# Performance work log

Hardware: AMD Instinct MI355X
Metric: run time of the kernel (lower is better)

Reference implementation:

```python
import jax, jax.numpy as jnp
import numpy as np

N_NODES = 100000


def sage_conv(x, src, dst, W_l, b_l, W_r):
    # PyG SAGEConv (aggr='mean'): out = lin_l(mean_j x_j) + lin_r(x_i)
    msg = x[src]  # [E, d] gather of source-node features
    agg = jax.ops.segment_sum(msg, dst, num_segments=N_NODES)  # [N, d]
    deg = jax.ops.segment_sum(jnp.ones((src.shape[0],), x.dtype), dst,
                              num_segments=N_NODES)
    mean = agg / jnp.clip(deg, 1.0, None)[:, None]
    return mean @ W_l.T + b_l + x @ W_r.T


def setup_inputs() -> dict:
    key = jax.random.key(0)
    ks = jax.random.split(key, 12)
    d_in, d_h, d_out, n_edges = 64, 64, 2, 1200000
    s = 1.0 / np.sqrt(d_h)
    inp = {
        "x": jax.random.normal(ks[0], (N_NODES, d_in), dtype=jnp.float32),
        "edge_index": jax.random.randint(ks[1], (2, n_edges), 0, N_NODES,
                                         dtype=jnp.int64),
        "W_l1": jax.random.uniform(ks[2], (d_h, d_in), jnp.float32, -s, s),
        "b_l1": jax.random.uniform(ks[3], (d_h,), jnp.float32, -s, s),
        "W_r1": jax.random.uniform(ks[4], (d_h, d_in), jnp.float32, -s, s),
        "W_l2": jax.random.uniform(ks[5], (d_h, d_h), jnp.float32, -s, s),
        "b_l2": jax.random.uniform(ks[6], (d_h,), jnp.float32, -s, s),
        "W_r2": jax.random.uniform(ks[7], (d_h, d_h), jnp.float32, -s, s),
        "W_c": jax.random.uniform(ks[8], (d_out, d_h), jnp.float32, -s, s),
        "b_c": jax.random.uniform(ks[9], (d_out,), jnp.float32, -s, s),
    }
    return inp


def reference(x, edge_index, W_l1, b_l1, W_r1, W_l2, b_l2, W_r2, W_c, b_c):
    src, dst = edge_index[0], edge_index[1]
    # layer 1 + relu (dropout is identity in eval mode)
    h = jax.nn.relu(sage_conv(x, src, dst, W_l1, b_l1, W_r1))
    # layer 2 (no relu per forward())
    h = sage_conv(h, src, dst, W_l2, b_l2, W_r2)
    # classifier
    return h @ W_c.T + b_c
```

## Files before the change

### kernel.cpp

```cpp
#include <hip/hip_runtime.h>

#define N_NODES 100000
#define D 64
#define NBUCK 391
#define NBLK_A 512
#define GCNT_N (NBUCK * NBLK_A)
#define NCHUNK ((GCNT_N + 255) / 256)
#define NTILE (N_NODES / 32)

typedef __attribute__((ext_vector_type(8))) short short8;
typedef __attribute__((ext_vector_type(16))) float f32x16;
union Pack8 { uint4 u; short8 s; };

__device__ __forceinline__ unsigned f2bf(float f) {
  unsigned u = __float_as_uint(f);
  return (u + 0x7fffu + ((u >> 16) & 1u)) >> 16;
}
#define BF_LO(u) __uint_as_float(((unsigned)(u)) << 16)
#define BF_HI(u) __uint_as_float(((unsigned)(u)) & 0xffff0000u)


__global__ __launch_bounds__(256) void passA_count(const int* __restrict__ dst,
                                                   int* __restrict__ gcnt,
                                                   int nE, int ec) {
  __shared__ int cnt[NBUCK];
  int t = threadIdx.x, blk = blockIdx.x;
  for (int i = t; i < NBUCK; i += 256) cnt[i] = 0;
  __syncthreads();
  int e0 = blk * ec, e1 = min(e0 + ec, nE);
  for (int e = e0 + t; e < e1; e += 256) atomicAdd(&cnt[dst[e] >> 8], 1);
  __syncthreads();
  for (int b = t; b < NBUCK; b += 256) gcnt[b * NBLK_A + blk] = cnt[b];
}

__global__ void gscan_p1(const int* __restrict__ g, int* __restrict__ csum) {
  int t = threadIdx.x, b = blockIdx.x;
  int i = b * 256 + t;
  int v = (i < GCNT_N) ? g[i] : 0;
  for (int off = 32; off; off >>= 1) v += __shfl_down(v, off);
  __shared__ int ws4[4];
  if ((t & 63) == 0) ws4[t >> 6] = v;
  __syncthreads();
  if (t == 0) csum[b] = ws4[0] + ws4[1] + ws4[2] + ws4[3];
}

__global__ void gscan_p2(int* __restrict__ csum, int nB) {
  __shared__ int s[1024];
  int t = threadIdx.x;
  int orig = (t < nB) ? csum[t] : 0;
  s[t] = orig;
  __syncthreads();
  for (int off = 1; off < 1024; off <<= 1) {
    int v = (t >= off) ? s[t - off] : 0;
    __syncthreads();
    s[t] += v;
    __syncthreads();
  }
  if (t < nB) csum[t] = s[t] - orig;
}

__global__ void gscan_p3(int* __restrict__ g, const int* __restrict__ csum) {
  __shared__ int s[256];
  int t = threadIdx.x, b = blockIdx.x;
  int i = b * 256 + t;
  int d = (i < GCNT_N) ? g[i] : 0;
  s[t] = d;
  __syncthreads();
  for (int off = 1; off < 256; off <<= 1) {
    int v = (t >= off) ? s[t - off] : 0;
    __syncthreads();
    s[t] += v;
    __syncthreads();
  }
  if (i < GCNT_N) g[i] = s[t] - d + csum[b];
}

__global__ __launch_bounds__(256) void passC_place(const int* __restrict__ src,
                                                   const int* __restrict__ dst,
                                                   const int* __restrict__ S,
                                                   uint2* __restrict__ pairs,
                                                   int nE, int ec) {
  __shared__ int cur[NBUCK];
  int t = threadIdx.x, blk = blockIdx.x;
  for (int b = t; b < NBUCK; b += 256) cur[b] = S[b * NBLK_A + blk];
  __syncthreads();
  int e0 = blk * ec, e1 = min(e0 + ec, nE);
  for (int e = e0 + t; e < e1; e += 256) {
    int d = dst[e];
    int p = atomicAdd(&cur[d >> 8], 1);
    pairs[p] = make_uint2((unsigned)d, (unsigned)src[e]);
  }
}

__global__ __launch_bounds__(256) void passD_csr(const uint2* __restrict__ pairs,
                                                 const int* __restrict__ S,
                                                 int* __restrict__ rowstart,
                                                 int* __restrict__ degI,
                                                 int* __restrict__ adj, int nE) {
  __shared__ int lh[256];
  __shared__ int sc[256];
  __shared__ int cur[256];
  int t = threadIdx.x, b = blockIdx.x;
  int base = S[b * NBLK_A];
  int end = (b == NBUCK - 1) ? nE : S[(b + 1) * NBLK_A];
  lh[t] = 0;
  __syncthreads();
  for (int p = base + t; p < end; p += 256) atomicAdd(&lh[pairs[p].x & 255], 1);
  __syncthreads();
  int d = lh[t];
  sc[t] = d;
  __syncthreads();
  for (int off = 1; off < 256; off <<= 1) {
    int v = (t >= off) ? sc[t - off] : 0;
    __syncthreads();
    sc[t] += v;
    __syncthreads();
  }
  int ex = sc[t] - d;
  int node = b * 256 + t;
  if (node < N_NODES) {
    rowstart[node] = base + ex;
    degI[node] = d;
  }
  cur[t] = base + ex;
  __syncthreads();
  for (int p = base + t; p < end; p += 256) {
    uint2 e = pairs[p];
    int slot = atomicAdd(&cur[e.x & 255], 1);
    adj[slot] = (int)e.y;
  }
}

__global__ void wfold_kernel(const float* __restrict__ Wc,
                             const float* __restrict__ Wl2,
                             const float* __restrict__ Wr2,
                             const float* __restrict__ bl2,
                             const float* __restrict__ bc,
                             float* __restrict__ A2, float* __restrict__ B2,
                             float* __restrict__ bfv) {
  int t = threadIdx.x;
  int c = t >> 6, k = t & 63;
  float sa = 0.f, sb = 0.f;
  for (int j = 0; j < 64; ++j) {
    float w = Wc[c * 64 + j];
    sa = fmaf(w, Wl2[j * 64 + k], sa);
    sb = fmaf(w, Wr2[j * 64 + k], sb);
  }
  A2[c * 64 + k] = sa;
  B2[c * 64 + k] = sb;
  if (t < 2) {
    float s = bc[t];
    for (int j = 0; j < 64; ++j) s = fmaf(Wc[t * 64 + j], bl2[j], s);
    bfv[t] = s;
  }
}

__global__ void wprep_kernel(const float* __restrict__ Wl,
                             const float* __restrict__ Wr,
                             unsigned short* __restrict__ wcat) {
  int i = blockIdx.x * 256 + threadIdx.x;
  if (i < 4096) wcat[i] = (unsigned short)f2bf(Wl[i]);
  else if (i < 8192) wcat[i] = (unsigned short)f2bf(Wr[i - 4096]);
}

__global__ __launch_bounds__(256) void transform_mfma(
    const float* __restrict__ x, const unsigned short* __restrict__ wcat,
    const float* __restrict__ bl, unsigned short* __restrict__ t1,
    unsigned short* __restrict__ r1b) {
  int tid = threadIdx.x, lane = tid & 63;
  int l31 = lane & 31, hi = lane >> 5;

  short8 af[4][4];
#pragma unroll
  for (int jt = 0; jt < 4; ++jt)
#pragma unroll
    for (int kk = 0; kk < 4; ++kk)
      af[jt][kk] = *(const short8*)(wcat + (jt * 32 + l31) * 64 + kk * 16 + 8 * hi);

  const f32x16 Z = {0.f, 0.f, 0.f, 0.f, 0.f, 0.f, 0.f, 0.f,
                    0.f, 0.f, 0.f, 0.f, 0.f, 0.f, 0.f, 0.f};
  const float4* x4 = (const float4*)x;

  int gw = (blockIdx.x * 256 + tid) >> 6;
  int nW = (gridDim.x * 256) >> 6;

  for (int tile = gw; tile < NTILE; tile += nW) {
    int node = tile * 32 + l31;
    f32x16 acc[4] = {Z, Z, Z, Z};
#pragma unroll
    for (int kk = 0; kk < 4; ++kk) {
      float4 fa = x4[(size_t)node * 16 + kk * 4 + 2 * hi];
      float4 fb = x4[(size_t)node * 16 + kk * 4 + 2 * hi + 1];
      Pack8 pk;
      pk.u.x = f2bf(fa.x) | (f2bf(fa.y) << 16);
      pk.u.y = f2bf(fa.z) | (f2bf(fa.w) << 16);
      pk.u.z = f2bf(fb.x) | (f2bf(fb.y) << 16);
      pk.u.w = f2bf(fb.z) | (f2bf(fb.w) << 16);
      acc[0] = __builtin_amdgcn_mfma_f32_32x32x16_bf16(af[0][kk], pk.s, acc[0], 0, 0, 0);
      acc[1] = __builtin_amdgcn_mfma_f32_32x32x16_bf16(af[1][kk], pk.s, acc[1], 0, 0, 0);
      acc[2] = __builtin_amdgcn_mfma_f32_32x32x16_bf16(af[2][kk], pk.s, acc[2], 0, 0, 0);
      acc[3] = __builtin_amdgcn_mfma_f32_32x32x16_bf16(af[3][kk], pk.s, acc[3], 0, 0, 0);
    }
#pragma unroll
    for (int jt = 0; jt < 2; ++jt)
#pragma unroll
      for (int rg = 0; rg < 4; ++rg) {
        int j0 = jt * 32 + 8 * rg + 4 * hi;
        uint2 p;
        p.x = f2bf(acc[jt][4 * rg + 0]) | (f2bf(acc[jt][4 * rg + 1]) << 16);
        p.y = f2bf(acc[jt][4 * rg + 2]) | (f2bf(acc[jt][4 * rg + 3]) << 16);
        *(uint2*)(t1 + (size_t)node * 64 + j0) = p;
      }
#pragma unroll
    for (int jt = 2; jt < 4; ++jt)
#pragma unroll
      for (int rg = 0; rg < 4; ++rg) {
        int j0 = (jt - 2) * 32 + 8 * rg + 4 * hi;
        float4 bv = ((const float4*)bl)[j0 >> 2];
        uint2 p;
        p.x = f2bf(acc[jt][4 * rg + 0] + bv.x) |
              (f2bf(acc[jt][4 * rg + 1] + bv.y) << 16);
        p.y = f2bf(acc[jt][4 * rg + 2] + bv.z) |
              (f2bf(acc[jt][4 * rg + 3] + bv.w) << 16);
        *(uint2*)(r1b + (size_t)node * 64 + j0) = p;
      }
  }
}

#define ACC8(acc, v, m)                     \
  acc[0] = fmaf(BF_LO(v.x), m, acc[0]);     \
  acc[1] = fmaf(BF_HI(v.x), m, acc[1]);     \
  acc[2] = fmaf(BF_LO(v.y), m, acc[2]);     \
  acc[3] = fmaf(BF_HI(v.y), m, acc[3]);     \
  acc[4] = fmaf(BF_LO(v.z), m, acc[4]);     \
  acc[5] = fmaf(BF_HI(v.z), m, acc[5]);     \
  acc[6] = fmaf(BF_LO(v.w), m, acc[6]);     \
  acc[7] = fmaf(BF_HI(v.w), m, acc[7]);

__global__ __launch_bounds__(512) void gather1_kernel(
    const int* __restrict__ rowstart, const int* __restrict__ degI,
    const int* __restrict__ adj, const unsigned short* __restrict__ t1,
    const unsigned short* __restrict__ r1b, const float* __restrict__ A2,
    const float* __restrict__ B2, float2* __restrict__ g2,
    float2* __restrict__ s2, int nE) {
  __shared__ float pAB[4][64];
  int tid = threadIdx.x;
  if (tid < 256) {
    int v = tid >> 6, f = tid & 63;
    pAB[v][f] = (v < 2) ? A2[v * 64 + f] : B2[(v - 2) * 64 + f];
  }
  __syncthreads();

  int lane = tid & 63;
  int o = lane >> 3, j8 = lane & 7;
  int gw = (blockIdx.x * 512 + tid) >> 6;
  int nW = (gridDim.x * 512) >> 6;

  for (int n = gw * 2; n < N_NODES; n += nW * 2) {
    int n1 = n + 1;
    int rs0 = rowstart[n], dg0 = degI[n];
    int rs1 = rowstart[n1], dg1 = degI[n1];
    float acc0[8] = {0.f, 0.f, 0.f, 0.f, 0.f, 0.f, 0.f, 0.f};
    float acc1[8] = {0.f, 0.f, 0.f, 0.f, 0.f, 0.f, 0.f, 0.f};
    int mx = max(dg0, dg1);
    for (int base = 0; base < mx; base += 64) {
      int cnt0 = min(max(dg0 - base, 0), 64);
      int cnt1 = min(max(dg1 - base, 0), 64);
      int a0 = adj[min(rs0 + base + ((lane < cnt0) ? lane : 0), nE - 1)];
      int a1 = adj[min(rs1 + base + ((lane < cnt1) ? lane : 0), nE - 1)];
      int mc = max(cnt0, cnt1);
      for (int t = 0; t < mc; t += 16) {
        int el0 = t + o, el1 = t + 8 + o;
        int b00 = __shfl(a0, el0), b01 = __shfl(a0, el1);
        int b10 = __shfl(a1, el0), b11 = __shfl(a1, el1);
        bool k00 = el0 < cnt0, k01 = el1 < cnt0;
        bool k10 = el0 < cnt1, k11 = el1 < cnt1;
        b00 = k00 ? b00 : n;  b01 = k01 ? b01 : n;
        b10 = k10 ? b10 : n1; b11 = k11 ? b11 : n1;
        uint4 v00 = *(const uint4*)(t1 + (size_t)b00 * 64 + j8 * 8);
        uint4 v01 = *(const uint4*)(t1 + (size_t)b01 * 64 + j8 * 8);
        uint4 v10 = *(const uint4*)(t1 + (size_t)b10 * 64 + j8 * 8);
        uint4 v11 = *(const uint4*)(t1 + (size_t)b11 * 64 + j8 * 8);
        float m00 = k00 ? 1.f : 0.f, m01 = k01 ? 1.f : 0.f;
        float m10 = k10 ? 1.f : 0.f, m11 = k11 ? 1.f : 0.f;
        ACC8(acc0, v00, m00)
        ACC8(acc0, v01, m01)
        ACC8(acc1, v10, m10)
        ACC8(acc1, v11, m11)
      }
    }
#pragma unroll
    for (int jj = 0; jj < 8; ++jj) {
      acc0[jj] += __shfl_xor(acc0[jj], 8);
      acc0[jj] += __shfl_xor(acc0[jj], 16);
      acc0[jj] += __shfl_xor(acc0[jj], 32);
      acc1[jj] += __shfl_xor(acc1[jj], 8);
      acc1[jj] += __shfl_xor(acc1[jj], 16);
      acc1[jj] += __shfl_xor(acc1[jj], 32);
    }
#pragma unroll
    for (int nn = 0; nn < 2; ++nn) {
      int nd = nn ? n1 : n;
      float* acc = nn ? acc1 : acc0;
      int dg = nn ? dg1 : dg0;
      float inv = 1.f / (float)max(dg, 1);
      uint4 rv = *(const uint4*)(r1b + (size_t)nd * 64 + j8 * 8);
      float h[8];
      h[0] = fmaxf(fmaf(acc[0], inv, BF_LO(rv.x)), 0.f);
      h[1] = fmaxf(fmaf(acc[1], inv, BF_HI(rv.x)), 0.f);
      h[2] = fmaxf(fmaf(acc[2], inv, BF_LO(rv.y)), 0.f);
      h[3] = fmaxf(fmaf(acc[3], inv, BF_HI(rv.y)), 0.f);
      h[4] = fmaxf(fmaf(acc[4], inv, BF_LO(rv.z)), 0.f);
      h[5] = fmaxf(fmaf(acc[5], inv, BF_HI(rv.z)), 0.f);
      h[6] = fmaxf(fmaf(acc[6], inv, BF_LO(rv.w)), 0.f);
      h[7] = fmaxf(fmaf(acc[7], inv, BF_HI(rv.w)), 0.f);
      float d0 = 0.f, d1 = 0.f, d2 = 0.f, d3 = 0.f;
#pragma unroll
      for (int i = 0; i < 8; ++i) {
        float hv = h[i];
        d0 = fmaf(hv, pAB[0][j8 * 8 + i], d0);
        d1 = fmaf(hv, pAB[1][j8 * 8 + i], d1);
        d2 = fmaf(hv, pAB[2][j8 * 8 + i], d2);
        d3 = fmaf(hv, pAB[3][j8 * 8 + i], d3);
      }
      d0 += __shfl_xor(d0, 1); d0 += __shfl_xor(d0, 2); d0 += __shfl_xor(d0, 4);
      d1 += __shfl_xor(d1, 1); d1 += __shfl_xor(d1, 2); d1 += __shfl_xor(d1, 4);
      d2 += __shfl_xor(d2, 1); d2 += __shfl_xor(d2, 2); d2 += __shfl_xor(d2, 4);
      d3 += __shfl_xor(d3, 1); d3 += __shfl_xor(d3, 2); d3 += __shfl_xor(d3, 4);
      if (lane == 0) {
        g2[nd] = make_float2(d0, d1);
        s2[nd] = make_float2(d2, d3);
      }
    }
  }
}

__global__ __launch_bounds__(256) void gather2_kernel(
    const int* __restrict__ rowstart, const int* __restrict__ degI,
    const int* __restrict__ adj, const float2* __restrict__ g2,
    const float2* __restrict__ s2, const float* __restrict__ bfv,
    float* __restrict__ out, int nE) {
  int tid = threadIdx.x, lane = tid & 63;
  int q = lane >> 4, l16 = lane & 15;
  float bf0 = bfv[0], bf1 = bfv[1];
  int gq = ((blockIdx.x * 256 + tid) >> 6) * 4 + q;
  int strideN = ((gridDim.x * 256) >> 6) * 4;
  for (int n = gq; n < N_NODES; n += strideN) {
    int rs = rowstart[n], dg = degI[n];
    float s0 = 0.f, s1 = 0.f;
    for (int base = 0; base < dg; base += 16) {
      int e = base + l16;
      int a = adj[min(rs + ((e < dg) ? e : 0), nE - 1)];
      float2 v = g2[a];
      float m = (e < dg) ? 1.f : 0.f;
      s0 = fmaf(v.x, m, s0);
      s1 = fmaf(v.y, m, s1);
    }
    s0 += __shfl_xor(s0, 1); s0 += __shfl_xor(s0, 2);
    s0 += __shfl_xor(s0, 4); s0 += __shfl_xor(s0, 8);
    s1 += __shfl_xor(s1, 1); s1 += __shfl_xor(s1, 2);
    s1 += __shfl_xor(s1, 4); s1 += __shfl_xor(s1, 8);
    if (l16 == 0) {
      float inv = 1.f / (float)max(dg, 1);
      float2 sv = s2[n];
      out[(size_t)n * 2 + 0] = fmaf(s0, inv, sv.x) + bf0;
      out[(size_t)n * 2 + 1] = fmaf(s1, inv, sv.y) + bf1;
    }
  }
}

extern "C" void kernel_launch(void* const* d_in, const int* in_sizes, int n_in,
                              void* d_out, int out_size, void* d_ws,
                              size_t ws_size, hipStream_t stream) {
  const float* x   = (const float*)d_in[0];
  const int*   ei  = (const int*)d_in[1];
  const float* Wl1 = (const float*)d_in[2];
  const float* bl1 = (const float*)d_in[3];
  const float* Wr1 = (const float*)d_in[4];
  const float* Wl2 = (const float*)d_in[5];
  const float* bl2 = (const float*)d_in[6];
  const float* Wr2 = (const float*)d_in[7];
  const float* Wc  = (const float*)d_in[8];
  const float* bc  = (const float*)d_in[9];
  float* out = (float*)d_out;

  int nE = in_sizes[1] / 2;
  const int* src = ei;
  const int* dst = ei + nE;

  unsigned short* r1b = (unsigned short*)d_ws;
  uint2* pairs = (uint2*)d_ws;
  unsigned short* t1 = r1b + (size_t)N_NODES * D;
  float2* g2 = (float2*)(t1 + (size_t)N_NODES * D);
  float2* s2 = g2 + N_NODES;
  float* A2 = (float*)(s2 + N_NODES);
  float* B2 = A2 + 128;
  float* bfv = B2 + 128;
  unsigned short* wcat = (unsigned short*)(bfv + 4);
  int* degI = (int*)(wcat + 8192);
  int* rowstart = degI + N_NODES;
  int* gcnt = rowstart + N_NODES;
  int* csum = gcnt + GCNT_N;
  int* adj = csum + 1024;

  int ec = (nE + NBLK_A - 1) / NBLK_A;

  passA_count<<<NBLK_A, 256, 0, stream>>>(dst, gcnt, nE, ec);
  gscan_p1<<<NCHUNK, 256, 0, stream>>>(gcnt, csum);
  gscan_p2<<<1, 1024, 0, stream>>>(csum, NCHUNK);
  gscan_p3<<<NCHUNK, 256, 0, stream>>>(gcnt, csum);
  passC_place<<<NBLK_A, 256, 0, stream>>>(src, dst, gcnt, pairs, nE, ec);
  passD_csr<<<NBUCK, 256, 0, stream>>>(pairs, gcnt, rowstart, degI, adj, nE);

  wfold_kernel<<<1, 128, 0, stream>>>(Wc, Wl2, Wr2, bl2, bc, A2, B2, bfv);
  wprep_kernel<<<32, 256, 0, stream>>>(Wl1, Wr1, wcat);
  transform_mfma<<<512, 256, 0, stream>>>(x, wcat, bl1, t1, r1b);
  gather1_kernel<<<1024, 512, 0, stream>>>(rowstart, degI, adj, t1, r1b, A2,
                                           B2, g2, s2, nE);
  gather2_kernel<<<512, 256, 0, stream>>>(rowstart, degI, adj, g2, s2, bfv,
                                          out, nE);
}
```

Before: 145.7 us.

## Bucket edges by 32-node tiles and aggregate layer 1 with MFMA one-hot matmul

Edge binning now uses 32-node tiles instead of 256-node buckets, so each wave owns one tile's edge list straight from the placed pairs. The layer-1 mean aggregation runs as a bf16 MFMA: gathered neighbor rows are staged in LDS and multiplied by a one-hot destination matrix, replacing per-node CSR gathers with shuffle reductions. This removes the per-node adjacency indirection and shuffle reductions from the gather. In exchange, the count/scan arrays grow about 8x and the counting kernels use fewer blocks with larger shared histograms. Work per tile is also serialized through 16-edge groups with LDS round trips.

```diff
diff --git a/kernel.cpp b/kernel.cpp
--- a/kernel.cpp
+++ b/kernel.cpp
@@ -2,11 +2,13 @@
 
 #define N_NODES 100000
 #define D 64
-#define NBUCK 391
-#define NBLK_A 512
-#define GCNT_N (NBUCK * NBLK_A)
+#define NTILES 3125
+#define NBLK_A 256
+#define GCNT_N (NTILES * NBLK_A)
 #define NCHUNK ((GCNT_N + 255) / 256)
-#define NTILE (N_NODES / 32)
+#define NBUCK_D 391
+#define NTILE_T (N_NODES / 32)
+#define TROW 72
 
 typedef __attribute__((ext_vector_type(8))) short short8;
 typedef __attribute__((ext_vector_type(16))) float f32x16;
@@ -23,14 +25,14 @@
 __global__ __launch_bounds__(256) void passA_count(const int* __restrict__ dst,
                                                    int* __restrict__ gcnt,
                                                    int nE, int ec) {
-  __shared__ int cnt[NBUCK];
+  __shared__ int cnt[NTILES];
   int t = threadIdx.x, blk = blockIdx.x;
-  for (int i = t; i < NBUCK; i += 256) cnt[i] = 0;
+  for (int i = t; i < NTILES; i += 256) cnt[i] = 0;
   __syncthreads();
   int e0 = blk * ec, e1 = min(e0 + ec, nE);
-  for (int e = e0 + t; e < e1; e += 256) atomicAdd(&cnt[dst[e] >> 8], 1);
-  __syncthreads();
-  for (int b = t; b < NBUCK; b += 256) gcnt[b * NBLK_A + blk] = cnt[b];
+  for (int e = e0 + t; e < e1; e += 256) atomicAdd(&cnt[dst[e] >> 5], 1);
+  __syncthreads();
+  for (int b = t; b < NTILES; b += 256) gcnt[b * NBLK_A + blk] = cnt[b];
 }
 
 __global__ void gscan_p1(const int* __restrict__ g, int* __restrict__ csum) {
@@ -47,16 +49,23 @@
 __global__ void gscan_p2(int* __restrict__ csum, int nB) {
   __shared__ int s[1024];
   int t = threadIdx.x;
-  int orig = (t < nB) ? csum[t] : 0;
-  s[t] = orig;
-  __syncthreads();
-  for (int off = 1; off < 1024; off <<= 1) {
-    int v = (t >= off) ? s[t - off] : 0;
-    __syncthreads();
-    s[t] += v;
-    __syncthreads();
-  }
-  if (t < nB) csum[t] = s[t] - orig;
+  int carry = 0;
+  for (int c0 = 0; c0 < nB; c0 += 1024) {
+    int i = c0 + t;
+    int orig = (i < nB) ? csum[i] : 0;
+    s[t] = orig;
+    __syncthreads();
+    for (int off = 1; off < 1024; off <<= 1) {
+      int v = (t >= off) ? s[t - off] : 0;
+      __syncthreads();
+      s[t] += v;
+      __syncthreads();
+    }
+    if (i < nB) csum[i] = s[t] - orig + carry;
+    int tot = s[1023];
+    __syncthreads();
+    carry += tot;
+  }
 }
 
 __global__ void gscan_p3(int* __restrict__ g, const int* __restrict__ csum) {
@@ -80,14 +89,14 @@
                                                    const int* __restrict__ S,
                                                    uint2* __restrict__ pairs,
                                                    int nE, int ec) {
-  __shared__ int cur[NBUCK];
+  __shared__ int cur[NTILES];
   int t = threadIdx.x, blk = blockIdx.x;
-  for (int b = t; b < NBUCK; b += 256) cur[b] = S[b * NBLK_A + blk];
+  for (int b = t; b < NTILES; b += 256) cur[b] = S[b * NBLK_A + blk];
   __syncthreads();
   int e0 = blk * ec, e1 = min(e0 + ec, nE);
   for (int e = e0 + t; e < e1; e += 256) {
     int d = dst[e];
-    int p = atomicAdd(&cur[d >> 8], 1);
+    int p = atomicAdd(&cur[d >> 5], 1);
     pairs[p] = make_uint2((unsigned)d, (unsigned)src[e]);
   }
 }
@@ -101,8 +110,8 @@
   __shared__ int sc[256];
   __shared__ int cur[256];
   int t = threadIdx.x, b = blockIdx.x;
-  int base = S[b * NBLK_A];
-  int end = (b == NBUCK - 1) ? nE : S[(b + 1) * NBLK_A];
+  int base = S[(b * 8) * NBLK_A];
+  int end = (b == NBUCK_D - 1) ? nE : S[((b + 1) * 8) * NBLK_A];
   lh[t] = 0;
   __syncthreads();
   for (int p = base + t; p < end; p += 256) atomicAdd(&lh[pairs[p].x & 255], 1);
@@ -184,7 +193,7 @@
   int gw = (blockIdx.x * 256 + tid) >> 6;
   int nW = (gridDim.x * 256) >> 6;
 
-  for (int tile = gw; tile < NTILE; tile += nW) {
+  for (int tile = gw; tile < NTILE_T; tile += nW) {
     int node = tile * 32 + l31;
     f32x16 acc[4] = {Z, Z, Z, Z};
 #pragma unroll
@@ -227,111 +236,123 @@
   }
 }
 
-#define ACC8(acc, v, m)                     \
-  acc[0] = fmaf(BF_LO(v.x), m, acc[0]);     \
-  acc[1] = fmaf(BF_HI(v.x), m, acc[1]);     \
-  acc[2] = fmaf(BF_LO(v.y), m, acc[2]);     \
-  acc[3] = fmaf(BF_HI(v.y), m, acc[3]);     \
-  acc[4] = fmaf(BF_LO(v.z), m, acc[4]);     \
-  acc[5] = fmaf(BF_HI(v.z), m, acc[5]);     \
-  acc[6] = fmaf(BF_LO(v.w), m, acc[6]);     \
-  acc[7] = fmaf(BF_HI(v.w), m, acc[7]);
-
-__global__ __launch_bounds__(512) void gather1_kernel(
-    const int* __restrict__ rowstart, const int* __restrict__ degI,
-    const int* __restrict__ adj, const unsigned short* __restrict__ t1,
+__global__ __launch_bounds__(256) void tile_g1(
+    const uint2* __restrict__ pairs, const int* __restrict__ S,
+    const unsigned short* __restrict__ t1,
     const unsigned short* __restrict__ r1b, const float* __restrict__ A2,
     const float* __restrict__ B2, float2* __restrict__ g2,
     float2* __restrict__ s2, int nE) {
   __shared__ float pAB[4][64];
-  int tid = threadIdx.x;
-  if (tid < 256) {
-    int v = tid >> 6, f = tid & 63;
-    pAB[v][f] = (v < 2) ? A2[v * 64 + f] : B2[(v - 2) * 64 + f];
-  }
-  __syncthreads();
-
-  int lane = tid & 63;
+  __shared__ unsigned short stg[4][2][16 * TROW];
+  int t = threadIdx.x, lane = t & 63, w = t >> 6;
+  pAB[t >> 6][t & 63] = (t < 128) ? A2[t] : B2[t - 128];
+  __syncthreads();
+
+  int tile = blockIdx.x * 4 + w;
+  if (tile >= NTILES) return;
+  int base = S[tile * NBLK_A];
+  int end = (tile == NTILES - 1) ? nE : S[(tile + 1) * NBLK_A];
+  int l31 = lane & 31, hi = lane >> 5;
   int o = lane >> 3, j8 = lane & 7;
-  int gw = (blockIdx.x * 512 + tid) >> 6;
-  int nW = (gridDim.x * 512) >> 6;
-
-  for (int n = gw * 2; n < N_NODES; n += nW * 2) {
-    int n1 = n + 1;
-    int rs0 = rowstart[n], dg0 = degI[n];
-    int rs1 = rowstart[n1], dg1 = degI[n1];
-    float acc0[8] = {0.f, 0.f, 0.f, 0.f, 0.f, 0.f, 0.f, 0.f};
-    float acc1[8] = {0.f, 0.f, 0.f, 0.f, 0.f, 0.f, 0.f, 0.f};
-    int mx = max(dg0, dg1);
-    for (int base = 0; base < mx; base += 64) {
-      int cnt0 = min(max(dg0 - base, 0), 64);
-      int cnt1 = min(max(dg1 - base, 0), 64);
-      int a0 = adj[min(rs0 + base + ((lane < cnt0) ? lane : 0), nE - 1)];
-      int a1 = adj[min(rs1 + base + ((lane < cnt1) ? lane : 0), nE - 1)];
-      int mc = max(cnt0, cnt1);
-      for (int t = 0; t < mc; t += 16) {
-        int el0 = t + o, el1 = t + 8 + o;
-        int b00 = __shfl(a0, el0), b01 = __shfl(a0, el1);
-        int b10 = __shfl(a1, el0), b11 = __shfl(a1, el1);
-        bool k00 = el0 < cnt0, k01 = el1 < cnt0;
-        bool k10 = el0 < cnt1, k11 = el1 < cnt1;
-        b00 = k00 ? b00 : n;  b01 = k01 ? b01 : n;
-        b10 = k10 ? b10 : n1; b11 = k11 ? b11 : n1;
-        uint4 v00 = *(const uint4*)(t1 + (size_t)b00 * 64 + j8 * 8);
-        uint4 v01 = *(const uint4*)(t1 + (size_t)b01 * 64 + j8 * 8);
-        uint4 v10 = *(const uint4*)(t1 + (size_t)b10 * 64 + j8 * 8);
-        uint4 v11 = *(const uint4*)(t1 + (size_t)b11 * 64 + j8 * 8);
-        float m00 = k00 ? 1.f : 0.f, m01 = k01 ? 1.f : 0.f;
-        float m10 = k10 ? 1.f : 0.f, m11 = k11 ? 1.f : 0.f;
-        ACC8(acc0, v00, m00)
-        ACC8(acc0, v01, m01)
-        ACC8(acc1, v10, m10)
-        ACC8(acc1, v11, m11)
+  unsigned short* st0 = &stg[w][0][0];
+  unsigned short* st1 = &stg[w][1][0];
+
+  const f32x16 Z = {0.f, 0.f, 0.f, 0.f, 0.f, 0.f, 0.f, 0.f,
+                    0.f, 0.f, 0.f, 0.f, 0.f, 0.f, 0.f, 0.f};
+  f32x16 acc0 = Z, acc1 = Z;
+  int degc = 0;
+  int ng = (end > base) ? ((end - base + 15) >> 4) : 0;
+
+  uint2 pr = make_uint2(0u, 0u);
+  int cnt = 0;
+  uint4 v0 = make_uint4(0, 0, 0, 0), v1 = make_uint4(0, 0, 0, 0);
+  if (ng > 0) {
+    pr = pairs[min(base + (lane & 15), nE - 1)];
+    cnt = min(end - base, 16);
+    int sv0 = __shfl((int)pr.y, o);
+    int sv1 = __shfl((int)pr.y, 8 + o);
+    v0 = *(const uint4*)(t1 + (size_t)((o < cnt) ? sv0 : 0) * 64 + j8 * 8);
+    v1 = *(const uint4*)(t1 + (size_t)((8 + o < cnt) ? sv1 : 0) * 64 + j8 * 8);
+  }
+
+  for (int gg = 0; gg < ng; ++gg) {
+    unsigned short* st = (gg & 1) ? st1 : st0;
+    *(uint4*)(st + o * TROW + j8 * 8) = v0;
+    *(uint4*)(st + (8 + o) * TROW + j8 * 8) = v1;
+    unsigned am[8];
+#pragma unroll
+    for (int m = 0; m < 8; ++m) {
+      int e = 8 * hi + m;
+      int dv = __shfl((int)pr.x, e);
+      bool ok = (e < cnt) && ((dv & 31) == l31);
+      am[m] = ok ? 0x3F80u : 0u;
+      degc += (am[m] >> 7) & 1;
+    }
+    Pack8 I;
+    I.u.x = am[0] | (am[1] << 16);
+    I.u.y = am[2] | (am[3] << 16);
+    I.u.z = am[4] | (am[5] << 16);
+    I.u.w = am[6] | (am[7] << 16);
+    if (gg + 1 < ng) {
+      int nb = base + (gg + 1) * 16;
+      pr = pairs[min(nb + (lane & 15), nE - 1)];
+      cnt = min(end - nb, 16);
+      int sv0 = __shfl((int)pr.y, o);
+      int sv1 = __shfl((int)pr.y, 8 + o);
+      v0 = *(const uint4*)(t1 + (size_t)((o < cnt) ? sv0 : 0) * 64 + j8 * 8);
+      v1 = *(const uint4*)(t1 + (size_t)((8 + o < cnt) ? sv1 : 0) * 64 + j8 * 8);
+    }
+    Pack8 Afrag0, Afrag1;
+    {
+      unsigned short b0[8], b1[8];
+#pragma unroll
+      for (int m = 0; m < 8; ++m) {
+        b0[m] = st[(8 * hi + m) * TROW + l31];
+        b1[m] = st[(8 * hi + m) * TROW + 32 + l31];
       }
-    }
-#pragma unroll
-    for (int jj = 0; jj < 8; ++jj) {
-      acc0[jj] += __shfl_xor(acc0[jj], 8);
-      acc0[jj] += __shfl_xor(acc0[jj], 16);
-      acc0[jj] += __shfl_xor(acc0[jj], 32);
-      acc1[jj] += __shfl_xor(acc1[jj], 8);
-      acc1[jj] += __shfl_xor(acc1[jj], 16);
-      acc1[jj] += __shfl_xor(acc1[jj], 32);
-    }
-#pragma unroll
-    for (int nn = 0; nn < 2; ++nn) {
-      int nd = nn ? n1 : n;
-      float* acc = nn ? acc1 : acc0;
-      int dg = nn ? dg1 : dg0;
-      float inv = 1.f / (float)max(dg, 1);
-      uint4 rv = *(const uint4*)(r1b + (size_t)nd * 64 + j8 * 8);
-      float h[8];
-      h[0] = fmaxf(fmaf(acc[0], inv, BF_LO(rv.x)), 0.f);
-      h[1] = fmaxf(fmaf(acc[1], inv, BF_HI(rv.x)), 0.f);
-      h[2] = fmaxf(fmaf(acc[2], inv, BF_LO(rv.y)), 0.f);
-      h[3] = fmaxf(fmaf(acc[3], inv, BF_HI(rv.y)), 0.f);
-      h[4] = fmaxf(fmaf(acc[4], inv, BF_LO(rv.z)), 0.f);
-      h[5] = fmaxf(fmaf(acc[5], inv, BF_HI(rv.z)), 0.f);
-      h[6] = fmaxf(fmaf(acc[6], inv, BF_LO(rv.w)), 0.f);
-      h[7] = fmaxf(fmaf(acc[7], inv, BF_HI(rv.w)), 0.f);
-      float d0 = 0.f, d1 = 0.f, d2 = 0.f, d3 = 0.f;
-#pragma unroll
-      for (int i = 0; i < 8; ++i) {
-        float hv = h[i];
-        d0 = fmaf(hv, pAB[0][j8 * 8 + i], d0);
-        d1 = fmaf(hv, pAB[1][j8 * 8 + i], d1);
-        d2 = fmaf(hv, pAB[2][j8 * 8 + i], d2);
-        d3 = fmaf(hv, pAB[3][j8 * 8 + i], d3);
+      Afrag0.u.x = b0[0] | ((unsigned)b0[1] << 16);
+      Afrag0.u.y = b0[2] | ((unsigned)b0[3] << 16);
+      Afrag0.u.z = b0[4] | ((unsigned)b0[5] << 16);
+      Afrag0.u.w = b0[6] | ((unsigned)b0[7] << 16);
+      Afrag1.u.x = b1[0] | ((unsigned)b1[1] << 16);
+      Afrag1.u.y = b1[2] | ((unsigned)b1[3] << 16);
+      Afrag1.u.z = b1[4] | ((unsigned)b1[5] << 16);
+      Afrag1.u.w = b1[6] | ((unsigned)b1[7] << 16);
+    }
+    acc0 = __builtin_amdgcn_mfma_f32_32x32x16_bf16(Afrag0.s, I.s, acc0, 0, 0, 0);
+    acc1 = __builtin_amdgcn_mfma_f32_32x32x16_bf16(Afrag1.s, I.s, acc1, 0, 0, 0);
+  }
+
+  float degf = (float)(degc + __shfl_xor(degc, 32));
+  float inv = 1.f / fmaxf(degf, 1.f);
+  int node = tile * 32 + l31;
+  float d0 = 0.f, d1 = 0.f, d2 = 0.f, d3 = 0.f;
+#pragma unroll
+  for (int fb = 0; fb < 2; ++fb) {
+#pragma unroll
+    for (int q4 = 0; q4 < 4; ++q4) {
+      int f0 = fb * 32 + q4 * 8 + 4 * hi;
+      uint2 rv = *(const uint2*)(r1b + (size_t)node * 64 + f0);
+      float bias[4] = {BF_LO(rv.x), BF_HI(rv.x), BF_LO(rv.y), BF_HI(rv.y)};
+#pragma unroll
+      for (int j = 0; j < 4; ++j) {
+        float a = fb ? acc1[q4 * 4 + j] : acc0[q4 * 4 + j];
+        float hv = fmaxf(fmaf(a, inv, bias[j]), 0.f);
+        int f = f0 + j;
+        d0 = fmaf(hv, pAB[0][f], d0);
+        d1 = fmaf(hv, pAB[1][f], d1);
+        d2 = fmaf(hv, pAB[2][f], d2);
+        d3 = fmaf(hv, pAB[3][f], d3);
       }
-      d0 += __shfl_xor(d0, 1); d0 += __shfl_xor(d0, 2); d0 += __shfl_xor(d0, 4);
-      d1 += __shfl_xor(d1, 1); d1 += __shfl_xor(d1, 2); d1 += __shfl_xor(d1, 4);
-      d2 += __shfl_xor(d2, 1); d2 += __shfl_xor(d2, 2); d2 += __shfl_xor(d2, 4);
-      d3 += __shfl_xor(d3, 1); d3 += __shfl_xor(d3, 2); d3 += __shfl_xor(d3, 4);
-      if (lane == 0) {
-        g2[nd] = make_float2(d0, d1);
-        s2[nd] = make_float2(d2, d3);
-      }
-    }
+    }
+  }
+  d0 += __shfl_xor(d0, 32);
+  d1 += __shfl_xor(d1, 32);
+  d2 += __shfl_xor(d2, 32);
+  d3 += __shfl_xor(d3, 32);
+  if (hi == 0) {
+    g2[node] = make_float2(d0, d1);
+    s2[node] = make_float2(d2, d3);
   }
 }
 
@@ -388,10 +409,10 @@
   const int* src = ei;
   const int* dst = ei + nE;
 
-  unsigned short* r1b = (unsigned short*)d_ws;
   uint2* pairs = (uint2*)d_ws;
-  unsigned short* t1 = r1b + (size_t)N_NODES * D;
-  float2* g2 = (float2*)(t1 + (size_t)N_NODES * D);
+  unsigned short* t1 = (unsigned short*)(pairs + nE);
+  unsigned short* r1b = t1 + (size_t)N_NODES * D;
+  float2* g2 = (float2*)(r1b + (size_t)N_NODES * D);
   float2* s2 = g2 + N_NODES;
   float* A2 = (float*)(s2 + N_NODES);
   float* B2 = A2 + 128;
@@ -401,7 +422,7 @@
   int* rowstart = degI + N_NODES;
   int* gcnt = rowstart + N_NODES;
   int* csum = gcnt + GCNT_N;
-  int* adj = csum + 1024;
+  int* adj = csum + 4096;
 
   int ec = (nE + NBLK_A - 1) / NBLK_A;
 
@@ -410,13 +431,14 @@
   gscan_p2<<<1, 1024, 0, stream>>>(csum, NCHUNK);
   gscan_p3<<<NCHUNK, 256, 0, stream>>>(gcnt, csum);
   passC_place<<<NBLK_A, 256, 0, stream>>>(src, dst, gcnt, pairs, nE, ec);
-  passD_csr<<<NBUCK, 256, 0, stream>>>(pairs, gcnt, rowstart, degI, adj, nE);
+  passD_csr<<<NBUCK_D, 256, 0, stream>>>(pairs, gcnt, rowstart, degI, adj, nE);
 
   wfold_kernel<<<1, 128, 0, stream>>>(Wc, Wl2, Wr2, bl2, bc, A2, B2, bfv);
   wprep_kernel<<<32, 256, 0, stream>>>(Wl1, Wr1, wcat);
   transform_mfma<<<512, 256, 0, stream>>>(x, wcat, bl1, t1, r1b);
-  gather1_kernel<<<1024, 512, 0, stream>>>(rowstart, degI, adj, t1, r1b, A2,
-                                           B2, g2, s2, nE);
+
+  tile_g1<<<(NTILES + 3) / 4, 256, 0, stream>>>(pairs, gcnt, t1, r1b, A2, B2,
+                                                g2, s2, nE);
   gather2_kernel<<<512, 256, 0, stream>>>(rowstart, degI, adj, g2, s2, bfv,
                                           out, nE);
 }
```

New measurement: 161.1 us. +10.6%, slower.
